# Performance work log

Measured on AMD Instinct MI355X. Metric: run time of the kernel, lower is better.

The kernel has to match this reference:

```python
import jax, jax.numpy as jnp
import numpy as np

B, S, D, H = 2, 2048, 1024, 16
DK = D // H


def setup_inputs() -> dict:
    key = jax.random.key(0)
    ks = jax.random.split(key, 12)
    scale = 1.0 / np.sqrt(D)
    inp = {
        "query": jax.random.normal(ks[0], (B, S, D), jnp.float32),
        "key": jax.random.normal(ks[1], (B, S, D), jnp.float32),
        "value": jax.random.normal(ks[2], (B, S, D), jnp.float32),
        "mask": jnp.broadcast_to(jnp.tril(jnp.ones((S, S), bool)), (B, S, S)),
        "Wq": jax.random.normal(ks[3], (D, D), jnp.float32) * scale,
        "bq": jnp.zeros((D,), jnp.float32),
        "Wk": jax.random.normal(ks[4], (D, D), jnp.float32) * scale,
        "bk": jnp.zeros((D,), jnp.float32),
        "Wv": jax.random.normal(ks[5], (D, D), jnp.float32) * scale,
        "bv": jnp.zeros((D,), jnp.float32),
        "Wo": jax.random.normal(ks[6], (D, D), jnp.float32) * scale,
        "bo": jnp.zeros((D,), jnp.float32),
    }
    return inp


def _split_heads(x):
    # [B, S, D] -> [B, H, S, DK]
    return x.reshape(B, S, H, DK).transpose(0, 2, 1, 3)


def reference(query, key, value, mask, Wq, bq, Wk, bk, Wv, bv, Wo, bo):
    q = _split_heads(query @ Wq + bq)
    k = _split_heads(key @ Wk + bk)
    v = _split_heads(value @ Wv + bv)
    # scores: [B, H, S, S]
    scores = jnp.einsum("bhqd,bhkd->bhqk", q, k) / jnp.sqrt(jnp.float32(DK))
    scores = jnp.where(mask[:, None, :, :], scores, jnp.float32(-1e9))
    p_attn = jax.nn.softmax(scores, axis=-1)
    x = jnp.einsum("bhqk,bhkd->bhqd", p_attn, v)  # [B, H, S, DK]
    x = x.transpose(0, 2, 1, 3).reshape(B, S, D)
    return x @ Wo + bo
```

## Files before the change

### kernel.cpp

```cpp
#include <hip/hip_runtime.h>


#define S_LEN 2048
#define DMODEL 1024
#define NHEAD 16
#define DKH 64
#define QSCALE 0.18033688011112042f

typedef __attribute__((ext_vector_type(8))) short short8;
typedef __attribute__((ext_vector_type(4))) short short4v;
typedef __attribute__((ext_vector_type(4))) float f32x4;
typedef __attribute__((ext_vector_type(4))) unsigned short ushort4v;

__device__ __forceinline__ unsigned short f2bf(float f) {
  union { float f; unsigned int u; } v; v.f = f;
  unsigned int r = v.u + 0x7fffu + ((v.u >> 16) & 1u);
  return (unsigned short)(r >> 16);
}

__device__ __forceinline__ unsigned int cvtpk_bf16(float lo, float hi) {
  unsigned int d;
  asm("v_cvt_pk_bf16_f32 %0, %1, %2" : "=v"(d) : "v"(lo), "v"(hi));
  return d;
}

__device__ __forceinline__ void gload_lds16(const void* g, void* l) {
  __builtin_amdgcn_global_load_lds(
      (const __attribute__((address_space(1))) void*)g,
      (__attribute__((address_space(3))) void*)l, 16, 0, 0);
}

__global__ __launch_bounds__(256) void transpose_cast(const float* __restrict__ W,
                                                      unsigned short* __restrict__ Wt) {
  __shared__ float tile[32][33];
  const int tx = threadIdx.x, ty = threadIdx.y;
  const int c0 = blockIdx.x * 32, r0 = blockIdx.y * 32;
#pragma unroll
  for (int i = 0; i < 32; i += 8)
    tile[ty + i][tx] = W[(r0 + ty + i) * 1024 + c0 + tx];
  __syncthreads();
#pragma unroll
  for (int i = 0; i < 32; i += 8)
    Wt[(c0 + ty + i) * 1024 + r0 + tx] = f2bf(tile[tx][ty + i]);
}

__global__ __launch_bounds__(256) void cast3(const float* __restrict__ s0,
                                             const float* __restrict__ s1,
                                             const float* __restrict__ s2,
                                             unsigned short* __restrict__ d0,
                                             unsigned short* __restrict__ d1,
                                             unsigned short* __restrict__ d2) {
  const int z = blockIdx.y;
  const float* src = (z == 0) ? s0 : (z == 1) ? s1 : s2;
  unsigned short* dst = (z == 0) ? d0 : (z == 1) ? d1 : d2;
  const int i = (blockIdx.x * 256 + threadIdx.x) * 8;
  float4 a = *(const float4*)&src[i];
  float4 b = *(const float4*)&src[i + 4];
  unsigned short u[8];
  u[0] = f2bf(a.x); u[1] = f2bf(a.y); u[2] = f2bf(a.z); u[3] = f2bf(a.w);
  u[4] = f2bf(b.x); u[5] = f2bf(b.y); u[6] = f2bf(b.z); u[7] = f2bf(b.w);
  *(short8*)&dst[i] = *(short8*)u;
}

__global__ __launch_bounds__(256) void qkv_gemm(
    const unsigned short* Qc, const unsigned short* Kc, const unsigned short* Vc,
    const unsigned short* WtQ, const unsigned short* WtK, const unsigned short* WtV,
    const float* bq, const float* bk, const float* bv,
    unsigned short* Qw, unsigned short* Kw, unsigned short* Vtw) {
  __shared__ unsigned short Alds[2][4096];
  __shared__ unsigned short Blds[2][4096];
  const int z = blockIdx.z;
  const unsigned short* A  = (z == 0) ? Qc : (z == 1) ? Kc : Vc;
  const unsigned short* Wt = (z == 0) ? WtQ : (z == 1) ? WtK : WtV;
  const float* bias        = (z == 0) ? bq : (z == 1) ? bk : bv;

  const int tid = threadIdx.x;
  const int m0 = blockIdx.x * 128, n0 = blockIdx.y * 128;
  const int wid = tid >> 6, lane = tid & 63;
  const int lg = lane >> 4, lr = lane & 15;
  const int wr = (wid >> 1) * 64, wc = (wid & 1) * 64;
  const int srow_base = wid * 32 + (lane >> 2);
  const int scol = (lane & 3) * 8;

  f32x4 acc[4][4] = {};

#define GSTAGE(BUF, KT)                                                          \
  {                                                                              \
    _Pragma("unroll")                                                            \
    for (int i = 0; i < 2; i++) {                                                \
      const int row = srow_base + i * 16;                                        \
      gload_lds16(A  + (m0 + row) * 1024 + (KT) + scol,                          \
                  (char*)&Alds[BUF][0] + wid * 2048 + i * 1024);                 \
      gload_lds16(Wt + (n0 + row) * 1024 + (KT) + scol,                          \
                  (char*)&Blds[BUF][0] + wid * 2048 + i * 1024);                 \
    }                                                                            \
  }

  GSTAGE(0, 0)
  int cur = 0;
  for (int kt = 0; kt < 1024; kt += 32) {
    __syncthreads();
    if (kt + 32 < 1024) GSTAGE(cur ^ 1, kt + 32)
    short8 af[4], bfr[4];
#pragma unroll
    for (int i = 0; i < 4; i++) af[i] = *(short8*)&Alds[cur][(wr + i * 16 + lr) * 32 + lg * 8];
#pragma unroll
    for (int i = 0; i < 4; i++) bfr[i] = *(short8*)&Blds[cur][(wc + i * 16 + lr) * 32 + lg * 8];
#pragma unroll
    for (int mi = 0; mi < 4; mi++)
#pragma unroll
      for (int ni = 0; ni < 4; ni++)
        acc[mi][ni] = __builtin_amdgcn_mfma_f32_16x16x32_bf16(af[mi], bfr[ni], acc[mi][ni], 0, 0, 0);
    cur ^= 1;
  }
#undef GSTAGE

  if (z < 2) {
    unsigned short* O = (z == 0) ? Qw : Kw;
    const float sc = (z == 0) ? QSCALE : 1.0f;
#pragma unroll
    for (int mi = 0; mi < 4; mi++)
#pragma unroll
      for (int ni = 0; ni < 4; ni++) {
        const int gn = n0 + wc + ni * 16 + lr;
        const int h = gn >> 6, dk = gn & 63;
        const float bb = bias[gn];
#pragma unroll
        for (int r = 0; r < 4; r++) {
          const int gm = m0 + wr + mi * 16 + lg * 4 + r;
          const int b = gm >> 11, s = gm & 2047;
          O[(((b * NHEAD + h) * S_LEN + s) << 6) + dk] = f2bf((acc[mi][ni][r] + bb) * sc);
        }
      }
  } else {
#pragma unroll
    for (int mi = 0; mi < 4; mi++)
#pragma unroll
      for (int ni = 0; ni < 4; ni++) {
        const int gn = n0 + wc + ni * 16 + lr;
        const int h = gn >> 6, dk = gn & 63;
        const float bb = bias[gn];
        const int gm = m0 + wr + mi * 16 + lg * 4;
        const int b = gm >> 11, s = gm & 2047;
        unsigned short u[4];
#pragma unroll
        for (int r = 0; r < 4; r++) u[r] = f2bf(acc[mi][ni][r] + bb);
        *(ushort4v*)&Vtw[(((b * NHEAD + h) * DKH + dk) << 11) + s] = *(ushort4v*)u;
      }
  }
}

__global__ __launch_bounds__(256) void oproj_gemm(const unsigned short* __restrict__ A,
                                                  const unsigned short* __restrict__ Wt,
                                                  const float* __restrict__ bias,
                                                  float* __restrict__ Of32) {
  __shared__ unsigned short Alds[2][2048];
  __shared__ unsigned short Blds[2][4096];
  const int tid = threadIdx.x;
  const int m0 = blockIdx.x * 64, n0 = blockIdx.y * 128;
  const int wid = tid >> 6, lane = tid & 63;
  const int lg = lane >> 4, lr = lane & 15;
  const int wc = wid * 32;
  const int arow = wid * 16 + (lane >> 2);
  const int brow_base = wid * 32 + (lane >> 2);
  const int scol = (lane & 3) * 8;

  f32x4 acc[4][2] = {};

#define OSTAGE(BUF, KT)                                                          \
  {                                                                              \
    gload_lds16(A + (m0 + arow) * 1024 + (KT) + scol,                            \
                (char*)&Alds[BUF][0] + wid * 1024);                              \
    _Pragma("unroll")                                                            \
    for (int i = 0; i < 2; i++) {                                                \
      const int row = brow_base + i * 16;                                        \
      gload_lds16(Wt + (n0 + row) * 1024 + (KT) + scol,                          \
                  (char*)&Blds[BUF][0] + wid * 2048 + i * 1024);                 \
    }                                                                            \
  }

  OSTAGE(0, 0)
  int cur = 0;
  for (int kt = 0; kt < 1024; kt += 32) {
    __syncthreads();
    if (kt + 32 < 1024) OSTAGE(cur ^ 1, kt + 32)
    short8 af[4], bfr[2];
#pragma unroll
    for (int i = 0; i < 4; i++) af[i] = *(short8*)&Alds[cur][(i * 16 + lr) * 32 + lg * 8];
#pragma unroll
    for (int j = 0; j < 2; j++) bfr[j] = *(short8*)&Blds[cur][(wc + j * 16 + lr) * 32 + lg * 8];
#pragma unroll
    for (int mi = 0; mi < 4; mi++)
#pragma unroll
      for (int ni = 0; ni < 2; ni++)
        acc[mi][ni] = __builtin_amdgcn_mfma_f32_16x16x32_bf16(af[mi], bfr[ni], acc[mi][ni], 0, 0, 0);
    cur ^= 1;
  }
#undef OSTAGE

#pragma unroll
  for (int mi = 0; mi < 4; mi++)
#pragma unroll
    for (int ni = 0; ni < 2; ni++) {
      const int gn = n0 + wc + ni * 16 + lr;
      const float bb = bias[gn];
#pragma unroll
      for (int r = 0; r < 4; r++) {
        const int gm = m0 + mi * 16 + lg * 4 + r;
        Of32[gm * 1024 + gn] = acc[mi][ni][r] + bb;
      }
    }
}

__global__ __launch_bounds__(256) void attn_k(const unsigned short* __restrict__ Q,
                                              const unsigned short* __restrict__ K,
                                              const unsigned short* __restrict__ Vt,
                                              unsigned short* __restrict__ X) {
  __shared__ unsigned short Kb[2][4096];
  __shared__ unsigned short Vb[2][4096];
  const int tid = threadIdx.x;
  const int wid = tid >> 6, lane = tid & 63;
  const int lg = lane >> 4, lr = lane & 15;
  const int bh = blockIdx.y;
  const unsigned short* Qh = Q + bh * (S_LEN * DKH);
  const char* KhB = (const char*)(K + bh * (S_LEN * DKH));
  const char* VtB = (const char*)(Vt + bh * (DKH * S_LEN));
  const int b = bh >> 4, h = bh & 15;

  const int srow_lo = (lane >> 3);
  const int scolb = (lane & 7) * 16;

  short8 ones8;
#pragma unroll
  for (int i = 0; i < 8; i++) ones8[i] = (short)0x3F80;

  for (int pass = 0; pass < 2; ++pass) {
    const int qt = (pass == 0) ? (int)blockIdx.x : 31 - (int)blockIdx.x;
    const int qr = qt * 64 + wid * 16;

    short8 qf[2];
#pragma unroll
    for (int c = 0; c < 2; c++) qf[c] = *(const short8*)&Qh[(qr + lr) * 64 + c * 32 + lg * 8];

    f32x4 o[4] = {};
    f32x4 lsv = {};

    int cur = 0;
    __syncthreads();

#define STAGE(BUF, KV)                                                          \
    {                                                                           \
      _Pragma("unroll")                                                         \
      for (int i = 0; i < 2; i++) {                                             \
        const int row = wid * 16 + i * 8 + srow_lo;                             \
        const int sw = scolb ^ ((row & 7) << 4);                                \
        gload_lds16(KhB + ((KV) + row) * 128 + sw,                              \
                    (char*)&Kb[BUF][0] + wid * 2048 + i * 1024);                \
        gload_lds16(VtB + row * 4096 + (KV) * 2 + sw,                           \
                    (char*)&Vb[BUF][0] + wid * 2048 + i * 1024);                \
      }                                                                         \
    }

    STAGE(cur, 0);

    for (int t = 0; t <= qt; ++t) {
      __syncthreads();
      if (t < qt) STAGE(cur ^ 1, (t + 1) * 64);
      const bool diag = (t == qt);

      f32x4 sa[4] = {};
      __builtin_amdgcn_s_setprio(1);
#pragma unroll
      for (int jf = 0; jf < 4; jf++) {
        const int row = jf * 16 + lr;
#pragma unroll
        for (int c = 0; c < 2; c++) {
          const int cb = (c * 64 + lg * 16) ^ ((lr & 7) << 4);
          short8 kf = *(const short8*)((const char*)&Kb[cur][0] + row * 128 + cb);
          sa[jf] = __builtin_amdgcn_mfma_f32_16x16x32_bf16(kf, qf[c], sa[jf], 0, 0, 0);
        }
      }
      __builtin_amdgcn_s_setprio(0);

      float p[4][4];
      if (diag) {
        const int qloc = wid * 16 + lr;
#pragma unroll
        for (int jf = 0; jf < 4; jf++)
#pragma unroll
          for (int r = 0; r < 4; r++) {
            const float e = exp2f(sa[jf][r]);
            p[jf][r] = (jf * 16 + lg * 4 + r > qloc) ? 0.f : e;
          }
      } else {
#pragma unroll
        for (int jf = 0; jf < 4; jf++)
#pragma unroll
          for (int r = 0; r < 4; r++) p[jf][r] = exp2f(sa[jf][r]);
      }

      union { short8 v; unsigned int u[4]; } pk[2];
#pragma unroll
      for (int c = 0; c < 2; c++) {
        pk[c].u[0] = cvtpk_bf16(p[2 * c][0], p[2 * c][1]);
        pk[c].u[1] = cvtpk_bf16(p[2 * c][2], p[2 * c][3]);
        pk[c].u[2] = cvtpk_bf16(p[2 * c + 1][0], p[2 * c + 1][1]);
        pk[c].u[3] = cvtpk_bf16(p[2 * c + 1][2], p[2 * c + 1][3]);
      }

      __builtin_amdgcn_s_setprio(1);
#pragma unroll
      for (int f = 0; f < 4; f++) {
        const char* vrow = (const char*)&Vb[cur][0] + (f * 16 + lr) * 128;
        const int swz = (lr & 7) << 4;
#pragma unroll
        for (int c = 0; c < 2; c++) {
          union { short8 v; short4v h[2]; } vv;
          vv.h[0] = *(const short4v*)(vrow + ((c * 64 + lg * 8) ^ swz));
          vv.h[1] = *(const short4v*)(vrow + ((c * 64 + 32 + lg * 8) ^ swz));
          o[f] = __builtin_amdgcn_mfma_f32_16x16x32_bf16(pk[c].v, vv.v, o[f], 0, 0, 0);
        }
      }
#pragma unroll
      for (int c = 0; c < 2; c++)
        lsv = __builtin_amdgcn_mfma_f32_16x16x32_bf16(pk[c].v, ones8, lsv, 0, 0, 0);
      __builtin_amdgcn_s_setprio(0);
      cur ^= 1;
    }

#pragma unroll
    for (int r = 0; r < 4; r++) {
      const float inv = 1.f / lsv[r];
      const int q = qr + lg * 4 + r;
#pragma unroll
      for (int f = 0; f < 4; f++)
        X[(b * S_LEN + q) * DMODEL + h * DKH + f * 16 + lr] = f2bf(o[f][r] * inv);
    }
  }
#undef STAGE
}

extern "C" void kernel_launch(void* const* d_in, const int* in_sizes, int n_in,
                              void* d_out, int out_size, void* d_ws, size_t ws_size,
                              hipStream_t stream) {
  const float* query = (const float*)d_in[0];
  const float* key   = (const float*)d_in[1];
  const float* value = (const float*)d_in[2];
  const float* Wq = (const float*)d_in[4];
  const float* bq = (const float*)d_in[5];
  const float* Wk = (const float*)d_in[6];
  const float* bk = (const float*)d_in[7];
  const float* Wv = (const float*)d_in[8];
  const float* bv = (const float*)d_in[9];
  const float* Wo = (const float*)d_in[10];
  const float* bo = (const float*)d_in[11];
  float* out = (float*)d_out;

  unsigned short* ws = (unsigned short*)d_ws;
  unsigned short* WtQ = ws;
  unsigned short* WtK = ws + 1048576;
  unsigned short* WtV = ws + 2097152;
  unsigned short* WtO = ws + 3145728;
  unsigned short* Qw  = ws + 4194304;
  unsigned short* Kw  = ws + 8388608;
  unsigned short* Vtw = ws + 12582912;
  unsigned short* Xw  = ws + 16777216;
  unsigned short* Qc  = ws + 20971520;
  unsigned short* Kc  = ws + 25165824;
  unsigned short* Vc  = ws + 29360128;
  (void)in_sizes; (void)n_in; (void)out_size; (void)ws_size;

  dim3 tb(32, 8), tg(32, 32);
  transpose_cast<<<tg, tb, 0, stream>>>(Wq, WtQ);
  transpose_cast<<<tg, tb, 0, stream>>>(Wk, WtK);
  transpose_cast<<<tg, tb, 0, stream>>>(Wv, WtV);
  transpose_cast<<<tg, tb, 0, stream>>>(Wo, WtO);

  cast3<<<dim3(2048, 3), 256, 0, stream>>>(query, key, value, Qc, Kc, Vc);

  qkv_gemm<<<dim3(32, 8, 3), 256, 0, stream>>>(Qc, Kc, Vc, WtQ, WtK, WtV,
                                               bq, bk, bv, Qw, Kw, Vtw);

  attn_k<<<dim3(16, 32), 256, 0, stream>>>(Qw, Kw, Vtw, Xw);

  oproj_gemm<<<dim3(64, 8), 256, 0, stream>>>(Xw, WtO, bo, out);
}
```

Measured before the change: 140.8 us.

## Split attention into one query tile per block, permute V layout, merge transposes

```diff
diff --git a/kernel.cpp b/kernel.cpp
--- a/kernel.cpp
+++ b/kernel.cpp
@@ -8,7 +8,6 @@
 #define QSCALE 0.18033688011112042f
 
 typedef __attribute__((ext_vector_type(8))) short short8;
-typedef __attribute__((ext_vector_type(4))) short short4v;
 typedef __attribute__((ext_vector_type(4))) float f32x4;
 typedef __attribute__((ext_vector_type(4))) unsigned short ushort4v;
 
@@ -30,9 +29,15 @@
       (__attribute__((address_space(3))) void*)l, 16, 0, 0);
 }
 
-__global__ __launch_bounds__(256) void transpose_cast(const float* __restrict__ W,
-                                                      unsigned short* __restrict__ Wt) {
+__global__ __launch_bounds__(256) void transpose_cast4(
+    const float* __restrict__ W0, const float* __restrict__ W1,
+    const float* __restrict__ W2, const float* __restrict__ W3,
+    unsigned short* __restrict__ T0, unsigned short* __restrict__ T1,
+    unsigned short* __restrict__ T2, unsigned short* __restrict__ T3) {
   __shared__ float tile[32][33];
+  const int z = blockIdx.z;
+  const float* W = (z == 0) ? W0 : (z == 1) ? W1 : (z == 2) ? W2 : W3;
+  unsigned short* Wt = (z == 0) ? T0 : (z == 1) ? T1 : (z == 2) ? T2 : T3;
   const int tx = threadIdx.x, ty = threadIdx.y;
   const int c0 = blockIdx.x * 32, r0 = blockIdx.y * 32;
 #pragma unroll
@@ -142,10 +147,13 @@
         const float bb = bias[gn];
         const int gm = m0 + wr + mi * 16 + lg * 4;
         const int b = gm >> 11, s = gm & 2047;
+        const int s6 = s & 63;
+        const int np = (s & ~63) + ((s6 >> 5) << 5) + (((s6 >> 2) & 3) << 3) +
+                       (((s6 >> 4) & 1) << 2);
         unsigned short u[4];
 #pragma unroll
         for (int r = 0; r < 4; r++) u[r] = f2bf(acc[mi][ni][r] + bb);
-        *(ushort4v*)&Vtw[(((b * NHEAD + h) * DKH + dk) << 11) + s] = *(ushort4v*)u;
+        *(ushort4v*)&Vtw[(((b * NHEAD + h) * DKH + dk) << 11) + np] = *(ushort4v*)u;
       }
   }
 }
@@ -234,108 +242,103 @@
 #pragma unroll
   for (int i = 0; i < 8; i++) ones8[i] = (short)0x3F80;
 
-  for (int pass = 0; pass < 2; ++pass) {
-    const int qt = (pass == 0) ? (int)blockIdx.x : 31 - (int)blockIdx.x;
-    const int qr = qt * 64 + wid * 16;
-
-    short8 qf[2];
-#pragma unroll
-    for (int c = 0; c < 2; c++) qf[c] = *(const short8*)&Qh[(qr + lr) * 64 + c * 32 + lg * 8];
-
-    f32x4 o[4] = {};
-    f32x4 lsv = {};
-
-    int cur = 0;
+  const int qt = 31 - (int)blockIdx.x;
+  const int qr = qt * 64 + wid * 16;
+
+  short8 qf[2];
+#pragma unroll
+  for (int c = 0; c < 2; c++) qf[c] = *(const short8*)&Qh[(qr + lr) * 64 + c * 32 + lg * 8];
+
+  f32x4 o[4] = {};
+  f32x4 lsv = {};
+
+  int cur = 0;
+
+#define STAGE(BUF, KV)                                                          \
+  {                                                                             \
+    _Pragma("unroll")                                                           \
+    for (int i = 0; i < 2; i++) {                                               \
+      const int row = wid * 16 + i * 8 + srow_lo;                               \
+      const int sw = scolb ^ ((row & 7) << 4);                                  \
+      gload_lds16(KhB + ((KV) + row) * 128 + sw,                                \
+                  (char*)&Kb[BUF][0] + wid * 2048 + i * 1024);                  \
+      gload_lds16(VtB + row * 4096 + (KV) * 2 + sw,                             \
+                  (char*)&Vb[BUF][0] + wid * 2048 + i * 1024);                  \
+    }                                                                           \
+  }
+
+  STAGE(cur, 0);
+
+  for (int t = 0; t <= qt; ++t) {
     __syncthreads();
-
-#define STAGE(BUF, KV)                                                          \
-    {                                                                           \
-      _Pragma("unroll")                                                         \
-      for (int i = 0; i < 2; i++) {                                             \
-        const int row = wid * 16 + i * 8 + srow_lo;                             \
-        const int sw = scolb ^ ((row & 7) << 4);                                \
-        gload_lds16(KhB + ((KV) + row) * 128 + sw,                              \
-                    (char*)&Kb[BUF][0] + wid * 2048 + i * 1024);                \
-        gload_lds16(VtB + row * 4096 + (KV) * 2 + sw,                           \
-                    (char*)&Vb[BUF][0] + wid * 2048 + i * 1024);                \
-      }                                                                         \
-    }
-
-    STAGE(cur, 0);
-
-    for (int t = 0; t <= qt; ++t) {
-      __syncthreads();
-      if (t < qt) STAGE(cur ^ 1, (t + 1) * 64);
-      const bool diag = (t == qt);
-
-      f32x4 sa[4] = {};
-      __builtin_amdgcn_s_setprio(1);
-#pragma unroll
-      for (int jf = 0; jf < 4; jf++) {
-        const int row = jf * 16 + lr;
-#pragma unroll
-        for (int c = 0; c < 2; c++) {
-          const int cb = (c * 64 + lg * 16) ^ ((lr & 7) << 4);
-          short8 kf = *(const short8*)((const char*)&Kb[cur][0] + row * 128 + cb);
-          sa[jf] = __builtin_amdgcn_mfma_f32_16x16x32_bf16(kf, qf[c], sa[jf], 0, 0, 0);
+    if (t < qt) STAGE(cur ^ 1, (t + 1) * 64);
+    const bool diag = (t == qt);
+
+    f32x4 sa[4] = {};
+    __builtin_amdgcn_s_setprio(1);
+#pragma unroll
+    for (int jf = 0; jf < 4; jf++) {
+      const int row = jf * 16 + lr;
+#pragma unroll
+      for (int c = 0; c < 2; c++) {
+        const int cb = (c * 64 + lg * 16) ^ ((lr & 7) << 4);
+        short8 kf = *(const short8*)((const char*)&Kb[cur][0] + row * 128 + cb);
+        sa[jf] = __builtin_amdgcn_mfma_f32_16x16x32_bf16(kf, qf[c], sa[jf], 0, 0, 0);
+      }
+    }
+    __builtin_amdgcn_s_setprio(0);
+
+    float p[4][4];
+    if (diag) {
+      const int qloc = wid * 16 + lr;
+#pragma unroll
+      for (int jf = 0; jf < 4; jf++)
+#pragma unroll
+        for (int r = 0; r < 4; r++) {
+          const float e = exp2f(sa[jf][r]);
+          p[jf][r] = (jf * 16 + lg * 4 + r > qloc) ? 0.f : e;
         }
-      }
-      __builtin_amdgcn_s_setprio(0);
-
-      float p[4][4];
-      if (diag) {
-        const int qloc = wid * 16 + lr;
-#pragma unroll
-        for (int jf = 0; jf < 4; jf++)
-#pragma unroll
-          for (int r = 0; r < 4; r++) {
-            const float e = exp2f(sa[jf][r]);
-            p[jf][r] = (jf * 16 + lg * 4 + r > qloc) ? 0.f : e;
-          }
-      } else {
-#pragma unroll
-        for (int jf = 0; jf < 4; jf++)
-#pragma unroll
-          for (int r = 0; r < 4; r++) p[jf][r] = exp2f(sa[jf][r]);
-      }
-
-      union { short8 v; unsigned int u[4]; } pk[2];
+    } else {
+#pragma unroll
+      for (int jf = 0; jf < 4; jf++)
+#pragma unroll
+        for (int r = 0; r < 4; r++) p[jf][r] = exp2f(sa[jf][r]);
+    }
+
+    union { short8 v; unsigned int u[4]; } pk[2];
+#pragma unroll
+    for (int c = 0; c < 2; c++) {
+      pk[c].u[0] = cvtpk_bf16(p[2 * c][0], p[2 * c][1]);
+      pk[c].u[1] = cvtpk_bf16(p[2 * c][2], p[2 * c][3]);
+      pk[c].u[2] = cvtpk_bf16(p[2 * c + 1][0], p[2 * c + 1][1]);
+      pk[c].u[3] = cvtpk_bf16(p[2 * c + 1][2], p[2 * c + 1][3]);
+    }
+
+    __builtin_amdgcn_s_setprio(1);
+#pragma unroll
+    for (int f = 0; f < 4; f++) {
+      const char* vrow = (const char*)&Vb[cur][0] + (f * 16 + lr) * 128;
+      const int swz = (lr & 7) << 4;
 #pragma unroll
       for (int c = 0; c < 2; c++) {
-        pk[c].u[0] = cvtpk_bf16(p[2 * c][0], p[2 * c][1]);
-        pk[c].u[1] = cvtpk_bf16(p[2 * c][2], p[2 * c][3]);
-        pk[c].u[2] = cvtpk_bf16(p[2 * c + 1][0], p[2 * c + 1][1]);
-        pk[c].u[3] = cvtpk_bf16(p[2 * c + 1][2], p[2 * c + 1][3]);
-      }
-
-      __builtin_amdgcn_s_setprio(1);
-#pragma unroll
-      for (int f = 0; f < 4; f++) {
-        const char* vrow = (const char*)&Vb[cur][0] + (f * 16 + lr) * 128;
-        const int swz = (lr & 7) << 4;
-#pragma unroll
-        for (int c = 0; c < 2; c++) {
-          union { short8 v; short4v h[2]; } vv;
-          vv.h[0] = *(const short4v*)(vrow + ((c * 64 + lg * 8) ^ swz));
-          vv.h[1] = *(const short4v*)(vrow + ((c * 64 + 32 + lg * 8) ^ swz));
-          o[f] = __builtin_amdgcn_mfma_f32_16x16x32_bf16(pk[c].v, vv.v, o[f], 0, 0, 0);
-        }
-      }
-#pragma unroll
-      for (int c = 0; c < 2; c++)
-        lsv = __builtin_amdgcn_mfma_f32_16x16x32_bf16(pk[c].v, ones8, lsv, 0, 0, 0);
-      __builtin_amdgcn_s_setprio(0);
-      cur ^= 1;
-    }
-
-#pragma unroll
-    for (int r = 0; r < 4; r++) {
-      const float inv = 1.f / lsv[r];
-      const int q = qr + lg * 4 + r;
-#pragma unroll
-      for (int f = 0; f < 4; f++)
-        X[(b * S_LEN + q) * DMODEL + h * DKH + f * 16 + lr] = f2bf(o[f][r] * inv);
-    }
+        short8 vf = *(const short8*)(vrow + ((c * 64 + lg * 16) ^ swz));
+        o[f] = __builtin_amdgcn_mfma_f32_16x16x32_bf16(pk[c].v, vf, o[f], 0, 0, 0);
+      }
+    }
+#pragma unroll
+    for (int c = 0; c < 2; c++)
+      lsv = __builtin_amdgcn_mfma_f32_16x16x32_bf16(pk[c].v, ones8, lsv, 0, 0, 0);
+    __builtin_amdgcn_s_setprio(0);
+    cur ^= 1;
+  }
+
+#pragma unroll
+  for (int r = 0; r < 4; r++) {
+    const float inv = 1.f / lsv[r];
+    const int q = qr + lg * 4 + r;
+#pragma unroll
+    for (int f = 0; f < 4; f++)
+      X[(b * S_LEN + q) * DMODEL + h * DKH + f * 16 + lr] = f2bf(o[f][r] * inv);
   }
 #undef STAGE
 }
@@ -370,18 +373,15 @@
   unsigned short* Vc  = ws + 29360128;
   (void)in_sizes; (void)n_in; (void)out_size; (void)ws_size;
 
-  dim3 tb(32, 8), tg(32, 32);
-  transpose_cast<<<tg, tb, 0, stream>>>(Wq, WtQ);
-  transpose_cast<<<tg, tb, 0, stream>>>(Wk, WtK);
-  transpose_cast<<<tg, tb, 0, stream>>>(Wv, WtV);
-  transpose_cast<<<tg, tb, 0, stream>>>(Wo, WtO);
+  transpose_cast4<<<dim3(32, 32, 4), dim3(32, 8), 0, stream>>>(
+      Wq, Wk, Wv, Wo, WtQ, WtK, WtV, WtO);
 
   cast3<<<dim3(2048, 3), 256, 0, stream>>>(query, key, value, Qc, Kc, Vc);
 
   qkv_gemm<<<dim3(32, 8, 3), 256, 0, stream>>>(Qc, Kc, Vc, WtQ, WtK, WtV,
                                                bq, bk, bv, Qw, Kw, Vtw);
 
-  attn_k<<<dim3(16, 32), 256, 0, stream>>>(Qw, Kw, Vtw, Xw);
+  attn_k<<<dim3(32, 32), 256, 0, stream>>>(Qw, Kw, Vtw, Xw);
 
   oproj_gemm<<<dim3(64, 8), 256, 0, stream>>>(Xw, WtO, bo, out);
 }
```

Measured after the change: 146.0 us. 3.7% more time.
